# Kernel optimization log

Measured on AMD Instinct MI355X. Metric: run time of the kernel, lower is better.

The kernel has to match this reference:

```python
import jax, jax.numpy as jnp
import numpy as np

H_DIM = 1024
N_NODES = 50000


def setup_inputs() -> dict:
    key = jax.random.key(0)
    ks = jax.random.split(key, 8)
    a = 1.0 / np.sqrt(H_DIM).astype(np.float32)  # torch Linear default U(-1/sqrt(fan_in), 1/sqrt(fan_in))
    # scale activations by 0.1 so the double exp (exp of scores, then softmax) stays finite in fp32
    H = jax.random.normal(ks[0], (N_NODES, H_DIM), jnp.float32) * 0.1
    h_t = jax.random.normal(ks[1], (1, H_DIM), jnp.float32) * 0.1
    W0 = jax.random.uniform(ks[2], (H_DIM, H_DIM), jnp.float32, -a, a)
    b0 = jax.random.uniform(ks[3], (H_DIM,), jnp.float32, -a, a)
    W1 = jax.random.uniform(ks[4], (H_DIM, H_DIM), jnp.float32, -a, a)
    b1 = jax.random.uniform(ks[5], (H_DIM,), jnp.float32, -a, a)
    W2 = jax.random.uniform(ks[6], (H_DIM, H_DIM), jnp.float32, -a, a)
    b2 = jax.random.uniform(ks[7], (H_DIM,), jnp.float32, -a, a)
    return {"H": H, "h_t": h_t, "W0": W0, "b0": b0, "W1": W1, "b1": b1, "W2": W2, "b2": b2}


def reference(H, h_t, W0, b0, W1, b1, W2, b2):
    # query vector w_0(h_t): [1, h_dim]
    q = h_t @ W0.T + b0
    # per-node raw score node.h @ w_0(h_t).T, then exp (as in the original loop): [N]
    scores = jnp.exp((H @ q.T).squeeze(-1))
    # original applies softmax on top of the exp'd scores (double exp) -- faithful
    w = jax.nn.softmax(scores)
    # weighted sum of node states: [1, h_dim]
    e_s = (w @ H)[None, :]
    # tanh-gated projection
    return jnp.tanh(e_s @ W1.T + b1 + h_t @ W2.T + b2)
```

## Files before the change

kernel.cpp:

```cpp
#include <hip/hip_runtime.h>
#include <hip/hip_bf16.h>

#define D 1024

typedef unsigned int u32;
typedef __attribute__((ext_vector_type(4))) unsigned int u32x4;

__device__ __forceinline__ float bflo(u32 u) { return __uint_as_float(u << 16); }
__device__ __forceinline__ float bfhi(u32 u) { return __uint_as_float(u & 0xffff0000u); }
__device__ __forceinline__ float bf1(const void* p, int j) {
    unsigned short s = ((const unsigned short*)p)[j];
    return __uint_as_float(((u32)s) << 16);
}

__device__ __forceinline__ float waveReduceSum(float v) {
#pragma unroll
    for (int off = 32; off > 0; off >>= 1) v += __shfl_xor(v, off, 64);
    return v;
}

__global__ __launch_bounds__(256) void k_probe(const u32* __restrict__ htw,
                                               int* __restrict__ flag,
                                               float* __restrict__ L,
                                               float* __restrict__ e_s) {
    int tid = threadIdx.x;
    for (int k = tid; k < D; k += 256) e_s[k] = 0.f;
    if (tid == 0) *L = 0.f;
    __shared__ int cnt;
    if (tid == 0) cnt = 0;
    __syncthreads();
    if (tid < 64) {
        u32 w = htw[tid];
        u32 e = (w >> 7) & 0xFF;
        if (e >= 100 && e <= 126) atomicAdd(&cnt, 1);
    }
    __syncthreads();
    if (tid == 0) *flag = (cnt >= 56) ? 1 : 0;
}

__global__ __launch_bounds__(256) void k_q(const int* __restrict__ flag,
                                           const void* __restrict__ W0,
                                           const void* __restrict__ ht,
                                           const void* __restrict__ b0,
                                           float* __restrict__ q) {
    int wid = threadIdx.x >> 6, lane = threadIdx.x & 63;
    int j = blockIdx.x * 4 + wid;
    int isBf16 = *flag;
    float s = 0.f;
    if (isBf16) {
        const u32x4* wrow = (const u32x4*)((const __hip_bfloat16*)W0 + (size_t)j * D);
        const u32x4* hv = (const u32x4*)ht;
#pragma unroll
        for (int half = 0; half < 2; ++half) {
            u32x4 a = wrow[half * 64 + lane];
            u32x4 b = hv[half * 64 + lane];
#pragma unroll
            for (int t = 0; t < 4; ++t) {
                s += bflo(a[t]) * bflo(b[t]);
                s += bfhi(a[t]) * bfhi(b[t]);
            }
        }
    } else {
        const float4* wrow = (const float4*)((const float*)W0 + (size_t)j * D);
        const float4* hv = (const float4*)ht;
#pragma unroll
        for (int t = 0; t < 4; ++t) {
            float4 a = wrow[t * 64 + lane];
            float4 b = hv[t * 64 + lane];
            s += a.x * b.x + a.y * b.y + a.z * b.z + a.w * b.w;
        }
    }
    s = waveReduceSum(s);
    if (lane == 0) {
        float bias = isBf16 ? bf1(b0, j) : ((const float*)b0)[j];
        q[j] = s + bias;
    }
}

__global__ __launch_bounds__(512) void k_pass(const int* __restrict__ flag,
                                              const void* __restrict__ Hm,
                                              const float* __restrict__ q,
                                              float* __restrict__ e_s,
                                              float* __restrict__ Lp,
                                              int N, int totalWaves) {
    __shared__ float lacc[8][D];
    __shared__ float ll[8];
    int wid = threadIdx.x >> 6, lane = threadIdx.x & 63;
    int gw = blockIdx.x * 8 + wid;
    int isBf16 = *flag;

    int col[16];
    if (isBf16) {
#pragma unroll
        for (int j = 0; j < 8; ++j) {
            col[j] = lane * 8 + j;
            col[8 + j] = 512 + lane * 8 + j;
        }
    } else {
#pragma unroll
        for (int t = 0; t < 4; ++t)
#pragma unroll
            for (int u = 0; u < 4; ++u) col[t * 4 + u] = t * 256 + lane * 4 + u;
    }
    float qr[16];
#pragma unroll
    for (int j = 0; j < 16; ++j) qr[j] = q[col[j]];

    float l = 0.f;
    float acc[16];
#pragma unroll
    for (int j = 0; j < 16; ++j) acc[j] = 0.f;

    for (int r = gw; r < N; r += totalWaves) {
        float h[16];
        if (isBf16) {
            const u32x4* hr = (const u32x4*)((const __hip_bfloat16*)Hm + (size_t)r * D);
            u32x4 a = hr[lane];
            u32x4 b = hr[64 + lane];
#pragma unroll
            for (int t = 0; t < 4; ++t) {
                h[2 * t] = bflo(a[t]);     h[2 * t + 1] = bfhi(a[t]);
                h[8 + 2 * t] = bflo(b[t]); h[8 + 2 * t + 1] = bfhi(b[t]);
            }
        } else {
            const float4* hr = (const float4*)((const float*)Hm + (size_t)r * D);
#pragma unroll
            for (int t = 0; t < 4; ++t) {
                float4 a = hr[t * 64 + lane];
                h[t * 4 + 0] = a.x; h[t * 4 + 1] = a.y;
                h[t * 4 + 2] = a.z; h[t * 4 + 3] = a.w;
            }
        }
        float d = 0.f;
#pragma unroll
        for (int j = 0; j < 16; ++j) d += h[j] * qr[j];
        d = waveReduceSum(d);
        float p = __expf(__expf(d));
        l += p;
#pragma unroll
        for (int j = 0; j < 16; ++j) acc[j] += p * h[j];
    }

#pragma unroll
    for (int j = 0; j < 16; ++j) lacc[wid][col[j]] = acc[j];
    if (lane == 0) ll[wid] = l;
    __syncthreads();
    for (int k = threadIdx.x; k < D; k += 512) {
        float s = 0.f;
#pragma unroll
        for (int w = 0; w < 8; ++w) s += lacc[w][k];
        atomicAdd(&e_s[k], s);
    }
    if (threadIdx.x == 0) {
        float s = 0.f;
#pragma unroll
        for (int w = 0; w < 8; ++w) s += ll[w];
        atomicAdd(Lp, s);
    }
}

__global__ __launch_bounds__(256) void k_out(const int* __restrict__ flag,
                                             const void* __restrict__ W1,
                                             const void* __restrict__ b1,
                                             const void* __restrict__ W2,
                                             const void* __restrict__ b2,
                                             const void* __restrict__ ht,
                                             const float* __restrict__ e_s,
                                             const float* __restrict__ Lp,
                                             void* __restrict__ out) {
    int wid = threadIdx.x >> 6, lane = threadIdx.x & 63;
    int j = blockIdx.x * 4 + wid;
    int isBf16 = *flag;
    float s1 = 0.f, s2 = 0.f;
    if (isBf16) {
        const u32x4* w1r = (const u32x4*)((const __hip_bfloat16*)W1 + (size_t)j * D);
        const u32x4* w2r = (const u32x4*)((const __hip_bfloat16*)W2 + (size_t)j * D);
        const u32x4* hv = (const u32x4*)ht;
        int c0 = lane * 8;
#pragma unroll
        for (int half = 0; half < 2; ++half) {
            u32x4 a = w1r[half * 64 + lane];
            u32x4 b = w2r[half * 64 + lane];
            u32x4 hh = hv[half * 64 + lane];
            const float4* ev = (const float4*)(e_s + half * 512 + c0);
            float4 ea = ev[0], eb = ev[1];
            float e[8] = {ea.x, ea.y, ea.z, ea.w, eb.x, eb.y, eb.z, eb.w};
#pragma unroll
            for (int t = 0; t < 4; ++t) {
                s1 += bflo(a[t]) * e[2 * t] + bfhi(a[t]) * e[2 * t + 1];
                s2 += bflo(b[t]) * bflo(hh[t]) + bfhi(b[t]) * bfhi(hh[t]);
            }
        }
    } else {
        const float4* w1r = (const float4*)((const float*)W1 + (size_t)j * D);
        const float4* w2r = (const float4*)((const float*)W2 + (size_t)j * D);
        const float4* hv = (const float4*)ht;
        const float4* ev = (const float4*)e_s;
#pragma unroll
        for (int t = 0; t < 4; ++t) {
            float4 a = w1r[t * 64 + lane];
            float4 b = w2r[t * 64 + lane];
            float4 hh = hv[t * 64 + lane];
            float4 ee = ev[t * 64 + lane];
            s1 += a.x * ee.x + a.y * ee.y + a.z * ee.z + a.w * ee.w;
            s2 += b.x * hh.x + b.y * hh.y + b.z * hh.z + b.w * hh.w;
        }
    }
    s1 = waveReduceSum(s1);
    s2 = waveReduceSum(s2);
    if (lane == 0) {
        float bias1 = isBf16 ? bf1(b1, j) : ((const float*)b1)[j];
        float bias2 = isBf16 ? bf1(b2, j) : ((const float*)b2)[j];
        float r = tanhf(s1 / (*Lp) + bias1 + s2 + bias2);
        if (isBf16) ((__hip_bfloat16*)out)[j] = __float2bfloat16(r);
        else        ((float*)out)[j] = r;
    }
}

extern "C" void kernel_launch(void* const* d_in, const int* in_sizes, int n_in,
                              void* d_out, int out_size, void* d_ws, size_t ws_size,
                              hipStream_t stream) {
    const void* H  = d_in[0];
    const void* ht = d_in[1];
    const void* W0 = d_in[2];
    const void* b0 = d_in[3];
    const void* W1 = d_in[4];
    const void* b1 = d_in[5];
    const void* W2 = d_in[6];
    const void* b2 = d_in[7];
    int N = in_sizes[0] / D;

    float* wsf  = (float*)d_ws;
    int*   flag = (int*)wsf;
    float* L    = wsf + 1;
    float* q    = wsf + 64;
    float* e_s  = wsf + 64 + 1024;

    const int B = 512;

    k_probe<<<1, 256, 0, stream>>>((const u32*)ht, flag, L, e_s);
    k_q<<<256, 256, 0, stream>>>(flag, W0, ht, b0, q);
    k_pass<<<B, 512, 0, stream>>>(flag, H, q, e_s, L, N, B * 8);
    k_out<<<256, 256, 0, stream>>>(flag, W1, b1, W2, b2, ht, e_s, L, d_out);
}
```

Baseline: 301.1 us.

## Unroll row loop by two, tree-reduce dots, replace atomics with two-stage reduction

The main pass now handles two rows per iteration so both row loads are in flight together, and it computes the per-lane dot product as a tree instead of a serial chain. The global atomicAdd accumulation of e_s and L is replaced by per-block partial writes, which a new k_fin kernel then reduces. The probe kernel shrinks to a single wave and no longer zeroes the accumulators. The goal is more memory-level parallelism and no atomic contention, at the price of an extra launch and roughly 2 MB of workspace traffic for the partials.

```diff
diff --git a/kernel.cpp b/kernel.cpp
--- a/kernel.cpp
+++ b/kernel.cpp
@@ -19,23 +19,14 @@
     return v;
 }
 
-__global__ __launch_bounds__(256) void k_probe(const u32* __restrict__ htw,
-                                               int* __restrict__ flag,
-                                               float* __restrict__ L,
-                                               float* __restrict__ e_s) {
-    int tid = threadIdx.x;
-    for (int k = tid; k < D; k += 256) e_s[k] = 0.f;
-    if (tid == 0) *L = 0.f;
-    __shared__ int cnt;
-    if (tid == 0) cnt = 0;
-    __syncthreads();
-    if (tid < 64) {
-        u32 w = htw[tid];
-        u32 e = (w >> 7) & 0xFF;
-        if (e >= 100 && e <= 126) atomicAdd(&cnt, 1);
-    }
-    __syncthreads();
-    if (tid == 0) *flag = (cnt >= 56) ? 1 : 0;
+__global__ __launch_bounds__(64) void k_probe(const u32* __restrict__ htw,
+                                              int* __restrict__ flag) {
+    int lane = threadIdx.x;
+    u32 w = htw[lane];
+    u32 e = (w >> 7) & 0xFF;
+    float c = (e >= 100 && e <= 126) ? 1.f : 0.f;
+    c = waveReduceSum(c);
+    if (lane == 0) *flag = (c >= 56.f) ? 1 : 0;
 }
 
 __global__ __launch_bounds__(256) void k_q(const int* __restrict__ flag,
@@ -77,11 +68,44 @@
     }
 }
 
+__device__ __forceinline__ void loadRow(const void* __restrict__ Hm, int r,
+                                        int isBf16, int lane, float* h) {
+    if (isBf16) {
+        const u32x4* hr = (const u32x4*)((const __hip_bfloat16*)Hm + (size_t)r * D);
+        u32x4 a = hr[lane];
+        u32x4 b = hr[64 + lane];
+#pragma unroll
+        for (int t = 0; t < 4; ++t) {
+            h[2 * t] = bflo(a[t]);     h[2 * t + 1] = bfhi(a[t]);
+            h[8 + 2 * t] = bflo(b[t]); h[8 + 2 * t + 1] = bfhi(b[t]);
+        }
+    } else {
+        const float4* hr = (const float4*)((const float*)Hm + (size_t)r * D);
+#pragma unroll
+        for (int t = 0; t < 4; ++t) {
+            float4 a = hr[t * 64 + lane];
+            h[t * 4 + 0] = a.x; h[t * 4 + 1] = a.y;
+            h[t * 4 + 2] = a.z; h[t * 4 + 3] = a.w;
+        }
+    }
+}
+
+__device__ __forceinline__ float dotTree(const float* h, const float* qr) {
+    float p[16];
+#pragma unroll
+    for (int j = 0; j < 16; ++j) p[j] = h[j] * qr[j];
+#pragma unroll
+    for (int step = 1; step < 16; step <<= 1)
+#pragma unroll
+        for (int j = 0; j < 16; j += 2 * step) p[j] += p[j + step];
+    return p[0];
+}
+
 __global__ __launch_bounds__(512) void k_pass(const int* __restrict__ flag,
                                               const void* __restrict__ Hm,
                                               const float* __restrict__ q,
-                                              float* __restrict__ e_s,
-                                              float* __restrict__ Lp,
+                                              float* __restrict__ accp,
+                                              float* __restrict__ lvals,
                                               int N, int totalWaves) {
     __shared__ float lacc[8][D];
     __shared__ float ll[8];
@@ -92,10 +116,7 @@
     int col[16];
     if (isBf16) {
 #pragma unroll
-        for (int j = 0; j < 8; ++j) {
-            col[j] = lane * 8 + j;
-            col[8 + j] = 512 + lane * 8 + j;
-        }
+        for (int j = 0; j < 8; ++j) { col[j] = lane * 8 + j; col[8 + j] = 512 + lane * 8 + j; }
     } else {
 #pragma unroll
         for (int t = 0; t < 4; ++t)
@@ -111,51 +132,69 @@
 #pragma unroll
     for (int j = 0; j < 16; ++j) acc[j] = 0.f;
 
-    for (int r = gw; r < N; r += totalWaves) {
-        float h[16];
-        if (isBf16) {
-            const u32x4* hr = (const u32x4*)((const __hip_bfloat16*)Hm + (size_t)r * D);
-            u32x4 a = hr[lane];
-            u32x4 b = hr[64 + lane];
-#pragma unroll
-            for (int t = 0; t < 4; ++t) {
-                h[2 * t] = bflo(a[t]);     h[2 * t + 1] = bfhi(a[t]);
-                h[8 + 2 * t] = bflo(b[t]); h[8 + 2 * t + 1] = bfhi(b[t]);
-            }
-        } else {
-            const float4* hr = (const float4*)((const float*)Hm + (size_t)r * D);
-#pragma unroll
-            for (int t = 0; t < 4; ++t) {
-                float4 a = hr[t * 64 + lane];
-                h[t * 4 + 0] = a.x; h[t * 4 + 1] = a.y;
-                h[t * 4 + 2] = a.z; h[t * 4 + 3] = a.w;
-            }
-        }
-        float d = 0.f;
-#pragma unroll
-        for (int j = 0; j < 16; ++j) d += h[j] * qr[j];
-        d = waveReduceSum(d);
-        float p = __expf(__expf(d));
-        l += p;
-#pragma unroll
-        for (int j = 0; j < 16; ++j) acc[j] += p * h[j];
+    int r = gw;
+    for (; r + totalWaves < N; r += 2 * totalWaves) {
+        float h0[16], h1[16];
+        loadRow(Hm, r, isBf16, lane, h0);
+        loadRow(Hm, r + totalWaves, isBf16, lane, h1);
+        float d0 = dotTree(h0, qr);
+        float d1 = dotTree(h1, qr);
+        d0 = waveReduceSum(d0);
+        d1 = waveReduceSum(d1);
+        float p0 = __expf(__expf(d0));
+        float p1 = __expf(__expf(d1));
+        l += p0 + p1;
+#pragma unroll
+        for (int j = 0; j < 16; ++j) acc[j] += p0 * h0[j] + p1 * h1[j];
+    }
+    if (r < N) {
+        float h0[16];
+        loadRow(Hm, r, isBf16, lane, h0);
+        float d0 = waveReduceSum(dotTree(h0, qr));
+        float p0 = __expf(__expf(d0));
+        l += p0;
+#pragma unroll
+        for (int j = 0; j < 16; ++j) acc[j] += p0 * h0[j];
     }
 
 #pragma unroll
     for (int j = 0; j < 16; ++j) lacc[wid][col[j]] = acc[j];
     if (lane == 0) ll[wid] = l;
     __syncthreads();
+    float* dst = accp + (size_t)blockIdx.x * D;
     for (int k = threadIdx.x; k < D; k += 512) {
         float s = 0.f;
 #pragma unroll
         for (int w = 0; w < 8; ++w) s += lacc[w][k];
-        atomicAdd(&e_s[k], s);
+        dst[k] = s;
     }
     if (threadIdx.x == 0) {
         float s = 0.f;
 #pragma unroll
         for (int w = 0; w < 8; ++w) s += ll[w];
-        atomicAdd(Lp, s);
+        lvals[blockIdx.x] = s;
+    }
+}
+
+__global__ __launch_bounds__(256) void k_fin(const float* __restrict__ accp,
+                                             const float* __restrict__ lvals,
+                                             float* __restrict__ e_s,
+                                             float* __restrict__ Ls, int B) {
+    __shared__ float part[4][64];
+    int t = threadIdx.x, lane = t & 63, chunk = t >> 6;
+    int col = blockIdx.x * 64 + lane;
+    int rpc = B >> 2;
+    float s = 0.f;
+    for (int b = chunk * rpc; b < (chunk + 1) * rpc; ++b)
+        s += accp[(size_t)b * D + col];
+    part[chunk][lane] = s;
+    __syncthreads();
+    if (t < 64) e_s[col] = part[0][lane] + part[1][lane] + part[2][lane] + part[3][lane];
+    if (blockIdx.x == 0 && chunk == 3) {
+        float ls = 0.f;
+        for (int b = lane; b < B; b += 64) ls += lvals[b];
+        ls = waveReduceSum(ls);
+        if (lane == 0) *Ls = ls;
     }
 }
 
@@ -166,7 +205,7 @@
                                              const void* __restrict__ b2,
                                              const void* __restrict__ ht,
                                              const float* __restrict__ e_s,
-                                             const float* __restrict__ Lp,
+                                             const float* __restrict__ Ls,
                                              void* __restrict__ out) {
     int wid = threadIdx.x >> 6, lane = threadIdx.x & 63;
     int j = blockIdx.x * 4 + wid;
@@ -211,7 +250,7 @@
     if (lane == 0) {
         float bias1 = isBf16 ? bf1(b1, j) : ((const float*)b1)[j];
         float bias2 = isBf16 ? bf1(b2, j) : ((const float*)b2)[j];
-        float r = tanhf(s1 / (*Lp) + bias1 + s2 + bias2);
+        float r = tanhf(s1 / (*Ls) + bias1 + s2 + bias2);
         if (isBf16) ((__hip_bfloat16*)out)[j] = __float2bfloat16(r);
         else        ((float*)out)[j] = r;
     }
@@ -232,14 +271,18 @@
 
     float* wsf  = (float*)d_ws;
     int*   flag = (int*)wsf;
-    float* L    = wsf + 1;
+    float* Ls   = wsf + 1;
     float* q    = wsf + 64;
-    float* e_s  = wsf + 64 + 1024;
-
-    const int B = 512;
-
-    k_probe<<<1, 256, 0, stream>>>((const u32*)ht, flag, L, e_s);
+    float* e_s  = wsf + 1088;
+    float* lvals= wsf + 2112;
+    float* accp = wsf + 4096;
+
+    int B = 512;
+    while (B > 64 && ws_size < (size_t)(4096 + (size_t)B * D) * 4) B >>= 1;
+
+    k_probe<<<1, 64, 0, stream>>>((const u32*)ht, flag);
     k_q<<<256, 256, 0, stream>>>(flag, W0, ht, b0, q);
-    k_pass<<<B, 512, 0, stream>>>(flag, H, q, e_s, L, N, B * 8);
-    k_out<<<256, 256, 0, stream>>>(flag, W1, b1, W2, b2, ht, e_s, L, d_out);
-}
+    k_pass<<<B, 512, 0, stream>>>(flag, H, q, accp, lvals, N, B * 8);
+    k_fin<<<D / 64, 256, 0, stream>>>(accp, lvals, e_s, Ls, B);
+    k_out<<<256, 256, 0, stream>>>(flag, W1, b1, W2, b2, ht, e_s, Ls, d_out);
+}
```

Result: slower. 336.2 us (+11.7%).
